# Performance work log

Measured on AMD Instinct MI355X. Metric: run time of the kernel, lower is better.

Reference implementation:

```python
import jax, jax.numpy as jnp
import numpy as np

B, DIM_IN, T = 16, 512, 2048
DIM_OUT2 = 512 * 2  # dim_out * 2 (GLU halves it)
K = 3
STYLE = 128
SCALE_CONV = 1.0 / np.sqrt(DIM_IN * K ** 2).astype(np.float32)  # fan_in = dim_in * k^2 (as in source)
SCALE_LIN = 1.0 / np.sqrt(STYLE).astype(np.float32)


def setup_inputs() -> dict:
    key = jax.random.key(0)
    ks = jax.random.split(key, 6)
    x = jax.random.normal(ks[0], (B, DIM_IN, T), dtype=jnp.float32)
    c_src = jax.random.normal(ks[1], (B, STYLE), dtype=jnp.float32)
    c_trg = jax.random.normal(ks[2], (B, STYLE), dtype=jnp.float32)
    # EqualLinear params (lr_mul=1): weight ~ N(0,1), bias filled with bias_init=1
    w_s = jax.random.normal(ks[3], (DIM_IN, STYLE), dtype=jnp.float32)
    b_s = jnp.ones((DIM_IN,), dtype=jnp.float32)
    w_b = jax.random.normal(ks[4], (DIM_IN, STYLE), dtype=jnp.float32)
    b_b = jnp.ones((DIM_IN,), dtype=jnp.float32)
    weight = jax.random.normal(ks[5], (1, DIM_OUT2, DIM_IN, K), dtype=jnp.float32)
    return {"x": x, "c_src": c_src, "c_trg": c_trg,
            "w_s": w_s, "b_s": b_s, "w_b": w_b, "b_b": b_b, "weight": weight}


def reference(x, c_src, c_trg, w_s, b_s, w_b, b_b, weight):
    bsz, cin, t = x.shape
    cout = weight.shape[1]  # dim_out * 2
    k = weight.shape[3]
    # EqualLinear: F.linear(c, w*scale, bias)
    s = (c_trg @ (w_s * SCALE_LIN).T + b_s).reshape(bsz, 1, cin, 1)
    beta = (c_trg @ (w_b * SCALE_LIN).T + b_b).reshape(bsz, 1, cin, 1)
    w = SCALE_CONV * (weight * s + beta)               # [B, Cout, Cin, K]
    demod = jax.lax.rsqrt(jnp.sum(w * w, axis=(2, 3)) + 1e-8)   # [B, Cout]
    demod_mean = jnp.mean(w.reshape(bsz, cout, -1), axis=2)      # [B, Cout]
    w = (w - demod_mean[:, :, None, None]) * demod[:, :, None, None]
    # batch-as-groups conv1d
    w = w.reshape(bsz * cout, cin, k)
    xr = x.reshape(1, bsz * cin, t)
    out = jax.lax.conv_general_dilated(
        xr, w, window_strides=(1,), padding=[(k // 2, k // 2)],
        dimension_numbers=("NCH", "OIH", "NCH"), feature_group_count=bsz)
    out = out.reshape(bsz, cout, -1)
    a, g = jnp.split(out, 2, axis=1)  # GLU on channel dim
    return a * jax.nn.sigmoid(g)
```

## Files before the change

### kernel.cpp

```cpp
#include <hip/hip_runtime.h>
#include <math.h>

typedef __attribute__((ext_vector_type(8))) short short8;
typedef __attribute__((ext_vector_type(4))) float f32x4;
typedef unsigned short ushortT;

#define NB     16
#define CIN    512
#define TT     2048
#define COUT2  1024
#define NSTYLE 128
#define KKTOT  1536
#define TPAD   2050
#define NKT    24

#define SCALE_LIN  0.088388347648318447f
#define SCALE_CONV 0.014731391274719736f

__device__ __forceinline__ ushortT f2bf(float f) {
  union { float f; unsigned u; } v; v.f = f;
  unsigned r = v.u + 0x7fffu + ((v.u >> 16) & 1u);
  return (ushortT)(r >> 16);
}

__device__ __forceinline__ void gload16(const void* g, void* l) {
  __builtin_amdgcn_global_load_lds(
      (const __attribute__((address_space(1))) void*)g,
      (__attribute__((address_space(3))) void*)l, 16, 0, 0);
}

__global__ void style_kernel(const float* __restrict__ c_trg,
                             const float* __restrict__ w_s, const float* __restrict__ b_s,
                             const float* __restrict__ w_b, const float* __restrict__ b_b,
                             float* __restrict__ s, float* __restrict__ beta,
                             ushortT* __restrict__ xT) {
  int gid = blockIdx.x * 256 + threadIdx.x;
  int b = gid >> 9, ci = gid & 511;
  const float* ct = c_trg + b * NSTYLE;
  const float* ws = w_s + ci * NSTYLE;
  const float* wb = w_b + ci * NSTYLE;
  float as = 0.f, ab = 0.f;
#pragma unroll 8
  for (int j = 0; j < NSTYLE; ++j) {
    float c = ct[j];
    as += c * ws[j];
    ab += c * wb[j];
  }
  s[gid]    = as * SCALE_LIN + b_s[ci];
  beta[gid] = ab * SCALE_LIN + b_b[ci];
  xT[(size_t)b * TPAD * CIN + ci] = 0;
  xT[((size_t)b * TPAD + TPAD - 1) * CIN + ci] = 0;
}

__global__ void xpose_kernel(const float* __restrict__ x, ushortT* __restrict__ xT) {
  int b = blockIdx.z, ct = blockIdx.y, tt = blockIdx.x;
  int t0 = tt * 64, ci0 = ct * 64;
  __shared__ float tile[64][65];
  const float* xB = x + (size_t)b * CIN * TT;
  int rr = threadIdx.x >> 4;
  int c4 = threadIdx.x & 15;
#pragma unroll
  for (int it = 0; it < 4; ++it) {
    int ci = rr + it * 16;
    float4 v = *(const float4*)(xB + (size_t)(ci0 + ci) * TT + t0 + c4 * 4);
    tile[ci][c4 * 4 + 0] = v.x; tile[ci][c4 * 4 + 1] = v.y;
    tile[ci][c4 * 4 + 2] = v.z; tile[ci][c4 * 4 + 3] = v.w;
  }
  __syncthreads();
  ushortT* xTB = xT + (size_t)b * TPAD * CIN;
#pragma unroll
  for (int it = 0; it < 4; ++it) {
    int t = rr + it * 16;
    ushort4 o;
    o.x = f2bf(tile[c4 * 4 + 0][t]); o.y = f2bf(tile[c4 * 4 + 1][t]);
    o.z = f2bf(tile[c4 * 4 + 2][t]); o.w = f2bf(tile[c4 * 4 + 3][t]);
    *(ushort4*)(xTB + (size_t)(1 + t0 + t) * CIN + ci0 + c4 * 4) = o;
  }
}

__global__ void modw_kernel(const float* __restrict__ weight,
                            const float* __restrict__ s, const float* __restrict__ beta,
                            ushortT* __restrict__ wnorm) {
  int co = blockIdx.x, b = blockIdx.y, tid = threadIdx.x;
  int ci = tid * 2;
  const float* wp = weight + (size_t)co * CIN * 3 + (size_t)ci * 3;
  float s0 = s[b * CIN + ci],     s1 = s[b * CIN + ci + 1];
  float e0 = beta[b * CIN + ci],  e1 = beta[b * CIN + ci + 1];
  float w0 = SCALE_CONV * (wp[0] * s0 + e0);
  float w1 = SCALE_CONV * (wp[1] * s0 + e0);
  float w2 = SCALE_CONV * (wp[2] * s0 + e0);
  float w3 = SCALE_CONV * (wp[3] * s1 + e1);
  float w4 = SCALE_CONV * (wp[4] * s1 + e1);
  float w5 = SCALE_CONV * (wp[5] * s1 + e1);
  float sum = w0 + w1 + w2 + w3 + w4 + w5;
  float sq  = w0*w0 + w1*w1 + w2*w2 + w3*w3 + w4*w4 + w5*w5;
#pragma unroll
  for (int off = 32; off; off >>= 1) {
    sum += __shfl_xor(sum, off);
    sq  += __shfl_xor(sq,  off);
  }
  __shared__ float rs[4], rq[4];
  if ((tid & 63) == 0) { rs[tid >> 6] = sum; rq[tid >> 6] = sq; }
  __syncthreads();
  float tsum = rs[0] + rs[1] + rs[2] + rs[3];
  float tsq  = rq[0] + rq[1] + rq[2] + rq[3];
  float mean  = tsum * (1.0f / 1536.0f);
  float demod = rsqrtf(tsq + 1e-8f);
  int r = ((co & 511) << 1) | (co >> 9);
  ushortT* dst = wnorm + ((size_t)b * COUT2 + r) * KKTOT;
  ushort2 p0, p1, p2;
  p0.x = f2bf((w0 - mean) * demod); p0.y = f2bf((w3 - mean) * demod);
  p1.x = f2bf((w1 - mean) * demod); p1.y = f2bf((w4 - mean) * demod);
  p2.x = f2bf((w2 - mean) * demod); p2.y = f2bf((w5 - mean) * demod);
  *(ushort2*)(dst +        ci) = p0;
  *(ushort2*)(dst +  512 + ci) = p1;
  *(ushort2*)(dst + 1024 + ci) = p2;
}


#define AFRAG(d, s, f) (*(const short8*)(ldsc + ((d) * 4 + (s)) * 16384 + aoff + (f) * 1024))
#define BFRAG(d, s, g) (*(const short8*)(ldsc + ((d) * 4 + 2 + (s)) * 16384 + boff + (g) * 1024))

#define RDA(as_, d, s, mh) do {              \
    as_##0 = AFRAG(d, s, (mh) * 4 + 0);      \
    as_##1 = AFRAG(d, s, (mh) * 4 + 1);      \
    as_##2 = AFRAG(d, s, (mh) * 4 + 2);      \
    as_##3 = AFRAG(d, s, (mh) * 4 + 3);      \
  } while (0)

#define RDB(bs_, d, s) do {                  \
    bs_##0 = BFRAG(d, s, 0);                 \
    bs_##1 = BFRAG(d, s, 1);                 \
    bs_##2 = BFRAG(d, s, 2);                 \
    bs_##3 = BFRAG(d, s, 3);                 \
  } while (0)

#define STAGE_A(d, s, kt) do {                                                   \
    int kc_ = (kt) * 64 + (s) * 32;                                              \
    gload16(wB + (size_t)(co0 + r0) * KKTOT + kc_ + jbs8,                        \
            ldsw + ((d) * 4 + (s)) * 8192 + tid * 8);                            \
    gload16(wB + (size_t)(co0 + r0 + 128) * KKTOT + kc_ + jbs8,                  \
            ldsw + ((d) * 4 + (s)) * 8192 + 4096 + tid * 8);                     \
  } while (0)

#define STAGE_B(d, s, kt) do {                                                   \
    int kc_ = (kt) * 64 + (s) * 32;                                              \
    int tap_ = kc_ >> 9; int ci_ = kc_ & 511;                                    \
    gload16(xB + (size_t)(t0 + r0 + tap_) * CIN + ci_ + jbs8,                    \
            ldsw + ((d) * 4 + 2 + (s)) * 8192 + tid * 8);                        \
    gload16(xB + (size_t)(t0 + r0 + 128 + tap_) * CIN + ci_ + jbs8,              \
            ldsw + ((d) * 4 + 2 + (s)) * 8192 + 4096 + tid * 8);                 \
  } while (0)

#define PHASE(mh, au_, bu_, RD_CODE, STAGES, ENDVM) do {                         \
    RD_CODE;                                                                     \
    STAGES;                                                                      \
    __builtin_amdgcn_sched_barrier(0);                                           \
    __builtin_amdgcn_s_barrier();                                                \
    __builtin_amdgcn_sched_barrier(0);                                           \
    __builtin_amdgcn_s_setprio(1);                                               \
    acc[(mh)*4+0][0] = __builtin_amdgcn_mfma_f32_16x16x32_bf16(au_##0, bu_##0, acc[(mh)*4+0][0], 0, 0, 0); \
    acc[(mh)*4+0][1] = __builtin_amdgcn_mfma_f32_16x16x32_bf16(au_##0, bu_##1, acc[(mh)*4+0][1], 0, 0, 0); \
    acc[(mh)*4+0][2] = __builtin_amdgcn_mfma_f32_16x16x32_bf16(au_##0, bu_##2, acc[(mh)*4+0][2], 0, 0, 0); \
    acc[(mh)*4+0][3] = __builtin_amdgcn_mfma_f32_16x16x32_bf16(au_##0, bu_##3, acc[(mh)*4+0][3], 0, 0, 0); \
    acc[(mh)*4+1][0] = __builtin_amdgcn_mfma_f32_16x16x32_bf16(au_##1, bu_##0, acc[(mh)*4+1][0], 0, 0, 0); \
    acc[(mh)*4+1][1] = __builtin_amdgcn_mfma_f32_16x16x32_bf16(au_##1, bu_##1, acc[(mh)*4+1][1], 0, 0, 0); \
    acc[(mh)*4+1][2] = __builtin_amdgcn_mfma_f32_16x16x32_bf16(au_##1, bu_##2, acc[(mh)*4+1][2], 0, 0, 0); \
    acc[(mh)*4+1][3] = __builtin_amdgcn_mfma_f32_16x16x32_bf16(au_##1, bu_##3, acc[(mh)*4+1][3], 0, 0, 0); \
    acc[(mh)*4+2][0] = __builtin_amdgcn_mfma_f32_16x16x32_bf16(au_##2, bu_##0, acc[(mh)*4+2][0], 0, 0, 0); \
    acc[(mh)*4+2][1] = __builtin_amdgcn_mfma_f32_16x16x32_bf16(au_##2, bu_##1, acc[(mh)*4+2][1], 0, 0, 0); \
    acc[(mh)*4+2][2] = __builtin_amdgcn_mfma_f32_16x16x32_bf16(au_##2, bu_##2, acc[(mh)*4+2][2], 0, 0, 0); \
    acc[(mh)*4+2][3] = __builtin_amdgcn_mfma_f32_16x16x32_bf16(au_##2, bu_##3, acc[(mh)*4+2][3], 0, 0, 0); \
    acc[(mh)*4+3][0] = __builtin_amdgcn_mfma_f32_16x16x32_bf16(au_##3, bu_##0, acc[(mh)*4+3][0], 0, 0, 0); \
    acc[(mh)*4+3][1] = __builtin_amdgcn_mfma_f32_16x16x32_bf16(au_##3, bu_##1, acc[(mh)*4+3][1], 0, 0, 0); \
    acc[(mh)*4+3][2] = __builtin_amdgcn_mfma_f32_16x16x32_bf16(au_##3, bu_##2, acc[(mh)*4+3][2], 0, 0, 0); \
    acc[(mh)*4+3][3] = __builtin_amdgcn_mfma_f32_16x16x32_bf16(au_##3, bu_##3, acc[(mh)*4+3][3], 0, 0, 0); \
    __builtin_amdgcn_s_setprio(0);                                               \
    __builtin_amdgcn_sched_barrier(0);                                           \
    if ((ENDVM) == 8)      asm volatile("s_waitcnt vmcnt(8)" ::: "memory");      \
    else if ((ENDVM) == 0) asm volatile("s_waitcnt vmcnt(0)" ::: "memory");      \
    __builtin_amdgcn_s_barrier();                                                \
    __builtin_amdgcn_sched_barrier(0);                                           \
  } while (0)

__global__ __launch_bounds__(512, 2)
void conv_gemm8(const ushortT* __restrict__ wnorm, const ushortT* __restrict__ xT,
                float* __restrict__ out) {
  extern __shared__ ushortT ldsw[];
  const char* ldsc = (const char*)ldsw;

  int orig = blockIdx.x;
  int wgid = (orig & 7) * 64 + (orig >> 3);
  int b  = wgid >> 5;
  int i5 = wgid & 31;
  int mp = i5 >> 4, r2 = i5 & 15;
  int nt = r2 >> 1, mt = mp * 2 + (r2 & 1);
  int co0 = mt * 256, t0 = nt * 256;

  int tid = threadIdx.x;
  int l = tid & 63, w = tid >> 6;
  int wm = w & 1, wn = w >> 1;

  int r0 = tid >> 2;
  int jbs8 = (((tid & 3) ^ ((r0 >> 1) & 3)) << 3);
  int cb = ((l >> 4) ^ ((l >> 1) & 3));
  int aoff = (wm * 128 + (l & 15)) * 64 + cb * 16;
  int boff = (wn * 64  + (l & 15)) * 64 + cb * 16;

  const ushortT* wB = wnorm + (size_t)b * COUT2 * KKTOT;
  const ushortT* xB = xT + (size_t)b * TPAD * CIN;

  f32x4 acc[8][4];
#pragma unroll
  for (int i = 0; i < 8; ++i)
#pragma unroll
    for (int j = 0; j < 4; ++j)
      acc[i][j] = (f32x4){0.f, 0.f, 0.f, 0.f};
  short8 ax0 = {}, ax1 = {}, ax2 = {}, ax3 = {};
  short8 ay0 = {}, ay1 = {}, ay2 = {}, ay3 = {};
  short8 bx0 = {}, bx1 = {}, bx2 = {}, bx3 = {};
  short8 by0 = {}, by1 = {}, by2 = {}, by3 = {};

  STAGE_A(0, 0, 0); STAGE_B(0, 0, 0); STAGE_A(0, 1, 0); STAGE_B(0, 1, 0);
  STAGE_B(1, 0, 1); STAGE_A(1, 0, 1); STAGE_B(1, 1, 1);
  asm volatile("s_waitcnt vmcnt(6)" ::: "memory");
  __builtin_amdgcn_sched_barrier(0);
  __builtin_amdgcn_s_barrier();
  __builtin_amdgcn_sched_barrier(0);
  RDA(ax, 0, 0, 0);
  RDB(bx, 0, 0);

  for (int j = 0; j < 11; ++j) {
    int kt1 = 2 * j + 1;
    int ktn0 = 2 * j + 2, ktn1 = 2 * j + 3;
    PHASE(0, ax, bx, { RDA(ay, 0, 0, 1); },                  STAGE_A(1, 1, kt1),   8);
    PHASE(1, ay, bx, { RDA(ax, 0, 1, 0); RDB(by, 0, 1); },   STAGE_B(0, 0, ktn0), -1);
    PHASE(0, ax, by, { RDA(ay, 0, 1, 1); },                  STAGE_A(0, 0, ktn0),  8);
    PHASE(1, ay, by, { RDA(ax, 1, 0, 0); RDB(bx, 1, 0); },   STAGE_B(0, 1, ktn0), -1);
    PHASE(0, ax, bx, { RDA(ay, 1, 0, 1); },                  STAGE_A(0, 1, ktn0),  8);
    PHASE(1, ay, bx, { RDA(ax, 1, 1, 0); RDB(by, 1, 1); },   STAGE_B(1, 0, ktn1), -1);
    PHASE(0, ax, by, { RDA(ay, 1, 1, 1); },                  STAGE_A(1, 0, ktn1),  8);
    PHASE(1, ay, by, { RDA(ax, 0, 0, 0); RDB(bx, 0, 0); },   STAGE_B(1, 1, ktn1), -1);
  }
  PHASE(0, ax, bx, { RDA(ay, 0, 0, 1); },                  STAGE_A(1, 1, 23),     0);
  PHASE(1, ay, bx, { RDA(ax, 0, 1, 0); RDB(by, 0, 1); },   {},                   -1);
  PHASE(0, ax, by, { RDA(ay, 0, 1, 1); },                  {},                   -1);
  PHASE(1, ay, by, { RDA(ax, 1, 0, 0); RDB(bx, 1, 0); },   {},                   -1);
  PHASE(0, ax, bx, { RDA(ay, 1, 0, 1); },                  {},                   -1);
  PHASE(1, ay, bx, { RDA(ax, 1, 1, 0); RDB(by, 1, 1); },   {},                   -1);
  PHASE(0, ax, by, { RDA(ay, 1, 1, 1); },                  {},                   -1);
  PHASE(1, ay, by, { },                                    {},                   -1);

#pragma unroll
  for (int f = 0; f < 8; ++f) {
    int cop = co0 + wm * 128 + f * 16 + ((l >> 4) << 2);
    int c = cop >> 1;
    size_t obase = ((size_t)b * (COUT2 / 2) + c) * TT;
#pragma unroll
    for (int g = 0; g < 4; ++g) {
      int t = t0 + wn * 64 + g * 16 + (l & 15);
      f32x4 v = acc[f][g];
      out[obase + t]      = v.x / (1.f + __expf(-v.y));
      out[obase + TT + t] = v.z / (1.f + __expf(-v.w));
    }
  }
}

extern "C" void kernel_launch(void* const* d_in, const int* in_sizes, int n_in,
                              void* d_out, int out_size, void* d_ws, size_t ws_size,
                              hipStream_t stream) {
  const float* x      = (const float*)d_in[0];
  const float* c_trg  = (const float*)d_in[2];
  const float* w_s    = (const float*)d_in[3];
  const float* b_s    = (const float*)d_in[4];
  const float* w_b    = (const float*)d_in[5];
  const float* b_b    = (const float*)d_in[6];
  const float* weight = (const float*)d_in[7];
  float* out = (float*)d_out;

  char* ws = (char*)d_ws;
  float*   s     = (float*)ws;
  float*   beta  = (float*)(ws + 32768);
  ushortT* xT    = (ushortT*)(ws + 65536);
  ushortT* wnorm = (ushortT*)(ws + 65536 + 33587200);

  hipFuncSetAttribute((const void*)conv_gemm8,
                      hipFuncAttributeMaxDynamicSharedMemorySize, 131072);

  style_kernel<<<32, 256, 0, stream>>>(c_trg, w_s, b_s, w_b, b_b, s, beta, xT);
  xpose_kernel<<<dim3(32, 8, 16), 256, 0, stream>>>(x, xT);
  modw_kernel<<<dim3(1024, 16), 256, 0, stream>>>(weight, s, beta, wnorm);
  conv_gemm8<<<512, 512, 131072, stream>>>(wnorm, xT, out);
}
```

Before: 136.4 us.

## Loop batches inside modw kernel and restructure GEMM phase barriers and waitcnts

The modulated-weight kernel now loads each output channel's weights once with vectorized float2 reads and loops over all 16 batches in one block, instead of launching one block per (channel, batch) that re-reads the weights. Separately, the GEMM phase macro changes from two barriers per phase to a single barrier at its start. The vmcnt waits drop to two points per unrolled iteration and sched_barriers are removed, which gives the compiler more freedom to interleave LDS reads, global loads and MFMAs. The looser synchronization risks LDS hazards if the new waitcnt accounting is wrong, and the modw kernel now has fewer, longer blocks.

```diff
diff --git a/kernel.cpp b/kernel.cpp
--- a/kernel.cpp
+++ b/kernel.cpp
@@ -81,40 +81,45 @@
 __global__ void modw_kernel(const float* __restrict__ weight,
                             const float* __restrict__ s, const float* __restrict__ beta,
                             ushortT* __restrict__ wnorm) {
-  int co = blockIdx.x, b = blockIdx.y, tid = threadIdx.x;
+  int co = blockIdx.x, tid = threadIdx.x;
   int ci = tid * 2;
-  const float* wp = weight + (size_t)co * CIN * 3 + (size_t)ci * 3;
-  float s0 = s[b * CIN + ci],     s1 = s[b * CIN + ci + 1];
-  float e0 = beta[b * CIN + ci],  e1 = beta[b * CIN + ci + 1];
-  float w0 = SCALE_CONV * (wp[0] * s0 + e0);
-  float w1 = SCALE_CONV * (wp[1] * s0 + e0);
-  float w2 = SCALE_CONV * (wp[2] * s0 + e0);
-  float w3 = SCALE_CONV * (wp[3] * s1 + e1);
-  float w4 = SCALE_CONV * (wp[4] * s1 + e1);
-  float w5 = SCALE_CONV * (wp[5] * s1 + e1);
-  float sum = w0 + w1 + w2 + w3 + w4 + w5;
-  float sq  = w0*w0 + w1*w1 + w2*w2 + w3*w3 + w4*w4 + w5*w5;
-#pragma unroll
-  for (int off = 32; off; off >>= 1) {
-    sum += __shfl_xor(sum, off);
-    sq  += __shfl_xor(sq,  off);
-  }
+  const float* wp = weight + (size_t)co * KKTOT + (size_t)ci * 3;
+  float2 va = *(const float2*)(wp);
+  float2 vb = *(const float2*)(wp + 2);
+  float2 vc = *(const float2*)(wp + 4);
+  float v0 = va.x, v1 = va.y, v2 = vb.x, v3 = vb.y, v4 = vc.x, v5 = vc.y;
+  int r = ((co & 511) << 1) | (co >> 9);
   __shared__ float rs[4], rq[4];
-  if ((tid & 63) == 0) { rs[tid >> 6] = sum; rq[tid >> 6] = sq; }
-  __syncthreads();
-  float tsum = rs[0] + rs[1] + rs[2] + rs[3];
-  float tsq  = rq[0] + rq[1] + rq[2] + rq[3];
-  float mean  = tsum * (1.0f / 1536.0f);
-  float demod = rsqrtf(tsq + 1e-8f);
-  int r = ((co & 511) << 1) | (co >> 9);
-  ushortT* dst = wnorm + ((size_t)b * COUT2 + r) * KKTOT;
-  ushort2 p0, p1, p2;
-  p0.x = f2bf((w0 - mean) * demod); p0.y = f2bf((w3 - mean) * demod);
-  p1.x = f2bf((w1 - mean) * demod); p1.y = f2bf((w4 - mean) * demod);
-  p2.x = f2bf((w2 - mean) * demod); p2.y = f2bf((w5 - mean) * demod);
-  *(ushort2*)(dst +        ci) = p0;
-  *(ushort2*)(dst +  512 + ci) = p1;
-  *(ushort2*)(dst + 1024 + ci) = p2;
+  for (int b = 0; b < NB; ++b) {
+    float2 sv = *(const float2*)(s + b * CIN + ci);
+    float2 ev = *(const float2*)(beta + b * CIN + ci);
+    float w0 = SCALE_CONV * (v0 * sv.x + ev.x);
+    float w1 = SCALE_CONV * (v1 * sv.x + ev.x);
+    float w2 = SCALE_CONV * (v2 * sv.x + ev.x);
+    float w3 = SCALE_CONV * (v3 * sv.y + ev.y);
+    float w4 = SCALE_CONV * (v4 * sv.y + ev.y);
+    float w5 = SCALE_CONV * (v5 * sv.y + ev.y);
+    float sum = w0 + w1 + w2 + w3 + w4 + w5;
+    float sq  = w0*w0 + w1*w1 + w2*w2 + w3*w3 + w4*w4 + w5*w5;
+#pragma unroll
+    for (int off = 32; off; off >>= 1) {
+      sum += __shfl_xor(sum, off);
+      sq  += __shfl_xor(sq,  off);
+    }
+    if ((tid & 63) == 0) { rs[tid >> 6] = sum; rq[tid >> 6] = sq; }
+    __syncthreads();
+    float mean  = (rs[0] + rs[1] + rs[2] + rs[3]) * (1.0f / 1536.0f);
+    float demod = rsqrtf(rq[0] + rq[1] + rq[2] + rq[3] + 1e-8f);
+    ushortT* dst = wnorm + ((size_t)b * COUT2 + r) * KKTOT;
+    ushort2 p0, p1, p2;
+    p0.x = f2bf((w0 - mean) * demod); p0.y = f2bf((w3 - mean) * demod);
+    p1.x = f2bf((w1 - mean) * demod); p1.y = f2bf((w4 - mean) * demod);
+    p2.x = f2bf((w2 - mean) * demod); p2.y = f2bf((w5 - mean) * demod);
+    *(ushort2*)(dst +        ci) = p0;
+    *(ushort2*)(dst +  512 + ci) = p1;
+    *(ushort2*)(dst + 1024 + ci) = p2;
+    __syncthreads();
+  }
 }
 
 
@@ -152,12 +157,13 @@
             ldsw + ((d) * 4 + 2 + (s)) * 8192 + 4096 + tid * 8);                 \
   } while (0)
 
-#define PHASE(mh, au_, bu_, RD_CODE, STAGES, ENDVM) do {                         \
+#define PHASE(mh, au_, bu_, RD_CODE, STAGES, VMN) do {                           \
+    if ((VMN) == 6)      asm volatile("s_waitcnt vmcnt(6)" ::: "memory");        \
+    else if ((VMN) == 4) asm volatile("s_waitcnt vmcnt(4)" ::: "memory");        \
+    else if ((VMN) == 0) asm volatile("s_waitcnt vmcnt(0)" ::: "memory");        \
+    __builtin_amdgcn_s_barrier();                                                \
     RD_CODE;                                                                     \
     STAGES;                                                                      \
-    __builtin_amdgcn_sched_barrier(0);                                           \
-    __builtin_amdgcn_s_barrier();                                                \
-    __builtin_amdgcn_sched_barrier(0);                                           \
     __builtin_amdgcn_s_setprio(1);                                               \
     acc[(mh)*4+0][0] = __builtin_amdgcn_mfma_f32_16x16x32_bf16(au_##0, bu_##0, acc[(mh)*4+0][0], 0, 0, 0); \
     acc[(mh)*4+0][1] = __builtin_amdgcn_mfma_f32_16x16x32_bf16(au_##0, bu_##1, acc[(mh)*4+0][1], 0, 0, 0); \
@@ -176,11 +182,6 @@
     acc[(mh)*4+3][2] = __builtin_amdgcn_mfma_f32_16x16x32_bf16(au_##3, bu_##2, acc[(mh)*4+3][2], 0, 0, 0); \
     acc[(mh)*4+3][3] = __builtin_amdgcn_mfma_f32_16x16x32_bf16(au_##3, bu_##3, acc[(mh)*4+3][3], 0, 0, 0); \
     __builtin_amdgcn_s_setprio(0);                                               \
-    __builtin_amdgcn_sched_barrier(0);                                           \
-    if ((ENDVM) == 8)      asm volatile("s_waitcnt vmcnt(8)" ::: "memory");      \
-    else if ((ENDVM) == 0) asm volatile("s_waitcnt vmcnt(0)" ::: "memory");      \
-    __builtin_amdgcn_s_barrier();                                                \
-    __builtin_amdgcn_sched_barrier(0);                                           \
   } while (0)
 
 __global__ __launch_bounds__(512, 2)
@@ -224,32 +225,30 @@
   STAGE_A(0, 0, 0); STAGE_B(0, 0, 0); STAGE_A(0, 1, 0); STAGE_B(0, 1, 0);
   STAGE_B(1, 0, 1); STAGE_A(1, 0, 1); STAGE_B(1, 1, 1);
   asm volatile("s_waitcnt vmcnt(6)" ::: "memory");
-  __builtin_amdgcn_sched_barrier(0);
   __builtin_amdgcn_s_barrier();
-  __builtin_amdgcn_sched_barrier(0);
   RDA(ax, 0, 0, 0);
   RDB(bx, 0, 0);
 
   for (int j = 0; j < 11; ++j) {
     int kt1 = 2 * j + 1;
-    int ktn0 = 2 * j + 2, ktn1 = 2 * j + 3;
-    PHASE(0, ax, bx, { RDA(ay, 0, 0, 1); },                  STAGE_A(1, 1, kt1),   8);
-    PHASE(1, ay, bx, { RDA(ax, 0, 1, 0); RDB(by, 0, 1); },   STAGE_B(0, 0, ktn0), -1);
-    PHASE(0, ax, by, { RDA(ay, 0, 1, 1); },                  STAGE_A(0, 0, ktn0),  8);
-    PHASE(1, ay, by, { RDA(ax, 1, 0, 0); RDB(bx, 1, 0); },   STAGE_B(0, 1, ktn0), -1);
-    PHASE(0, ax, bx, { RDA(ay, 1, 0, 1); },                  STAGE_A(0, 1, ktn0),  8);
-    PHASE(1, ay, bx, { RDA(ax, 1, 1, 0); RDB(by, 1, 1); },   STAGE_B(1, 0, ktn1), -1);
-    PHASE(0, ax, by, { RDA(ay, 1, 1, 1); },                  STAGE_A(1, 0, ktn1),  8);
-    PHASE(1, ay, by, { RDA(ax, 0, 0, 0); RDB(bx, 0, 0); },   STAGE_B(1, 1, ktn1), -1);
-  }
-  PHASE(0, ax, bx, { RDA(ay, 0, 0, 1); },                  STAGE_A(1, 1, 23),     0);
-  PHASE(1, ay, bx, { RDA(ax, 0, 1, 0); RDB(by, 0, 1); },   {},                   -1);
-  PHASE(0, ax, by, { RDA(ay, 0, 1, 1); },                  {},                   -1);
-  PHASE(1, ay, by, { RDA(ax, 1, 0, 0); RDB(bx, 1, 0); },   {},                   -1);
-  PHASE(0, ax, bx, { RDA(ay, 1, 0, 1); },                  {},                   -1);
-  PHASE(1, ay, bx, { RDA(ax, 1, 1, 0); RDB(by, 1, 1); },   {},                   -1);
-  PHASE(0, ax, by, { RDA(ay, 1, 1, 1); },                  {},                   -1);
-  PHASE(1, ay, by, { },                                    {},                   -1);
+    int k0n = 2 * j + 2, k1n = 2 * j + 3;
+    PHASE(0, ax, bx, { RDA(ay, 0, 0, 1); },                  STAGE_A(1, 1, kt1), -1);
+    PHASE(1, ay, bx, { RDA(ax, 0, 1, 0); RDB(by, 0, 1); },   STAGE_B(0, 0, k0n), -1);
+    PHASE(0, ax, by, { RDA(ay, 0, 1, 1); },                  STAGE_A(0, 0, k0n), -1);
+    PHASE(1, ay, by, { RDA(ax, 1, 0, 0); RDB(bx, 1, 0); },   STAGE_B(0, 1, k0n),  4);
+    PHASE(0, ax, bx, { RDA(ay, 1, 0, 1); },                  STAGE_A(0, 1, k0n), -1);
+    PHASE(1, ay, bx, { RDA(ax, 1, 1, 0); RDB(by, 1, 1); },   STAGE_B(1, 0, k1n), -1);
+    PHASE(0, ax, by, { RDA(ay, 1, 1, 1); },                  STAGE_A(1, 0, k1n), -1);
+    PHASE(1, ay, by, { RDA(ax, 0, 0, 0); RDB(bx, 0, 0); },   STAGE_B(1, 1, k1n),  4);
+  }
+  PHASE(0, ax, bx, { RDA(ay, 0, 0, 1); },                  STAGE_A(1, 1, 23), -1);
+  PHASE(1, ay, bx, { RDA(ax, 0, 1, 0); RDB(by, 0, 1); },   {},                -1);
+  PHASE(0, ax, by, { RDA(ay, 0, 1, 1); },                  {},                -1);
+  PHASE(1, ay, by, { RDA(ax, 1, 0, 0); RDB(bx, 1, 0); },   {},                 0);
+  PHASE(0, ax, bx, { RDA(ay, 1, 0, 1); },                  {},                -1);
+  PHASE(1, ay, bx, { RDA(ax, 1, 1, 0); RDB(by, 1, 1); },   {},                -1);
+  PHASE(0, ax, by, { RDA(ay, 1, 1, 1); },                  {},                -1);
+  PHASE(1, ay, by, { },                                    {},                -1);
 
 #pragma unroll
   for (int f = 0; f < 8; ++f) {
@@ -289,6 +288,6 @@
 
   style_kernel<<<32, 256, 0, stream>>>(c_trg, w_s, b_s, w_b, b_b, s, beta, xT);
   xpose_kernel<<<dim3(32, 8, 16), 256, 0, stream>>>(x, xT);
-  modw_kernel<<<dim3(1024, 16), 256, 0, stream>>>(weight, s, beta, wnorm);
+  modw_kernel<<<1024, 256, 0, stream>>>(weight, s, beta, wnorm);
   conv_gemm8<<<512, 512, 131072, stream>>>(wnorm, xT, out);
 }
```

After: 137.4 us. Within noise of the previous version (+0.8%).
